# Optimization experiments

Hardware: AMD Instinct MI355X
Metric: run time of the kernel (lower is better)

## Reference

```python
import jax, jax.numpy as jnp
import numpy as np

N_HEAD = 8
D_IN = 128
D_KEY = 32
B = 65536
EPS = 1e-5
TEMP = float(D_KEY ** 0.5)


def _xavier(k, shape):
    fan_out, fan_in = shape
    limit = float(np.sqrt(6.0 / (fan_in + fan_out)))
    return jax.random.uniform(k, shape, jnp.float32, -limit, limit)


def setup_inputs() -> dict:
    key = jax.random.key(0)
    ks = jax.random.split(key, 6)
    return {
        "h_emb": jax.random.normal(ks[0], (B, D_IN), jnp.float32),
        "r_emb": jax.random.normal(ks[1], (B, D_IN), jnp.float32),
        "w_h": _xavier(ks[2], (N_HEAD * D_IN, D_IN)),
        "w_r": _xavier(ks[3], (N_HEAD * D_IN, D_IN)),
        "k_h": _xavier(ks[4], (D_KEY, D_IN)),
        "k_r": _xavier(ks[5], (D_KEY, D_IN)),
        "ln_gamma": jnp.ones((D_IN,), jnp.float32),
        "ln_beta": jnp.zeros((D_IN,), jnp.float32),
        "mode": 0,  # 0 == 'normal'
    }


def reference(h_emb, r_emb, w_h, w_r, k_h, k_r, ln_gamma, ln_beta, mode):
    # mode == 0 <=> 'normal': h_batch = h_emb.shape[0], r_batch = r_emb.shape[0]
    residual = h_emb                                     # [B, D]
    hb = h_emb.shape[0]
    rb = r_emb.shape[0]
    # linear projections to n_head copies: [1, B, H, D]
    h1 = (h_emb @ w_h.T).reshape(-1, hb, N_HEAD, D_IN)
    r1 = (r_emb @ w_r.T).reshape(-1, rb, N_HEAD, D_IN)
    # small key projections: [1, B, H, K]
    h1k = h1 @ k_h.T
    r1k = r1 @ k_r.T
    # tiny HxH attention per batch element: [1, B, H, H]
    xattn = jnp.einsum('gbhk,gbjk->gbhj', h1k / TEMP, r1k)
    g, b = xattn.shape[0], xattn.shape[1]
    xattn = jax.nn.softmax(xattn.reshape(g, b, N_HEAD * N_HEAD), axis=-1)
    xattn = xattn.reshape(g, b, N_HEAD, N_HEAD)
    h_x = xattn.sum(axis=-1)[..., None]                  # [1, B, H, 1]
    r_x = xattn.sum(axis=-2)[..., None]                  # [1, B, H, 1]
    # weighted combine + head-sum + residual: [1, B, D]
    t = (h1 * h_x + r1 * r_x).sum(axis=-2) + residual
    # LayerNorm (applied because norm_flag is False in the original)
    mu = t.mean(axis=-1, keepdims=True)
    var = ((t - mu) ** 2).mean(axis=-1, keepdims=True)
    return ln_gamma * (t - mu) / jnp.sqrt(var + EPS) + ln_beta
```

## Files before the change

### kernel.cpp

```cpp
#include <hip/hip_runtime.h>
#include <hip/hip_fp16.h>

#define TEMP_INV 0.17677669529663687f

typedef _Float16 f16x8 __attribute__((ext_vector_type(8)));
typedef float    f32x4 __attribute__((ext_vector_type(4)));

__device__ __forceinline__ ushort f2h(float x){
  __half h = __float2half(x);
  return __half_as_ushort(h);
}
__device__ __forceinline__ ushort4 f4h(float4 v){
  ushort4 o; o.x=f2h(v.x); o.y=f2h(v.y); o.z=f2h(v.z); o.w=f2h(v.w); return o;
}
__device__ __forceinline__ f16x8 cvt8(float4 a, float4 b){
  f16x8 r;
  r[0]=(_Float16)a.x; r[1]=(_Float16)a.y; r[2]=(_Float16)a.z; r[3]=(_Float16)a.w;
  r[4]=(_Float16)b.x; r[5]=(_Float16)b.y; r[6]=(_Float16)b.z; r[7]=(_Float16)b.w;
  return r;
}
__device__ __forceinline__ f16x8 vscale(f16x8 v, _Float16 s){
  f16x8 r;
  #pragma unroll
  for (int i=0;i<8;i++) r[i] = v[i]*s;
  return r;
}

__global__ void prep_kernel(const float* __restrict__ wh, const float* __restrict__ wr,
                            const float* __restrict__ kh, const float* __restrict__ kr,
                            ushort* __restrict__ w16h, ushort* __restrict__ w16r,
                            ushort* __restrict__ cwh,  ushort* __restrict__ cwr){
  if (blockIdx.x < 128){
    int t = blockIdx.x * 256 + threadIdx.x;
    int R  = t >> 5;
    int c4 = t & 31;
    int h  = R >> 7, np = R & 127;
    int kq = c4 >> 1, pos = (c4 & 1) * 4;
    int dst = ((h*16 + kq)*128 + np)*8 + pos;
    float4 a = ((const float4*)wh)[t];
    *(ushort4*)&w16h[dst] = f4h(a);
    float4 b = ((const float4*)wr)[t];
    *(ushort4*)&w16r[dst] = f4h(b);
    return;
  }
  int bid = blockIdx.x - 128;
  int m  = bid >> 5;
  int h  = (bid >> 2) & 7;
  int iq = bid & 3;
  const float* w = m ? wr : wh;
  const float* k = m ? kr : kh;
  ushort* cw = m ? cwr : cwh;

  extern __shared__ char smem[];
  float* w_s = (float*)smem;
  float* k_s = w_s + 128*32;
  int t = threadIdx.x;

  #pragma unroll
  for (int p=0;p<4;p++){
    int f = t + p*256;
    int d = f >> 3, c4 = f & 7;
    *(float4*)&w_s[d*32 + c4*4] =
        *(const float4*)&w[(size_t)(h*128 + d)*128 + iq*32 + c4*4];
  }
  #pragma unroll
  for (int p=0;p<4;p++){
    int f = t + p*256;
    ((float4*)k_s)[f] = ((const float4*)k)[f];
  }
  __syncthreads();

  int il  = t & 31;
  int kk0 = t >> 5;
  float acc[4] = {0.f,0.f,0.f,0.f};
  for (int d=0; d<128; d++){
    float wv = w_s[d*32 + il];
    #pragma unroll
    for (int j=0;j<4;j++) acc[j] += k_s[(kk0 + 8*j)*128 + d] * wv;
  }
  int i = iq*32 + il;
  #pragma unroll
  for (int j=0;j<4;j++){
    int n = h*32 + kk0 + 8*j;
    cw[(size_t)((i>>3)*256 + n)*8 + (i&7)] = f2h(acc[j]);
  }
}

__global__ __launch_bounds__(256,4) void attn16_kernel(
    const float* __restrict__ h_emb, const float* __restrict__ r_emb,
    const ushort* __restrict__ cwh,  const ushort* __restrict__ cwr,
    float* __restrict__ hx, float* __restrict__ rx)
{
  __shared__ float hk[16*292];
  __shared__ float rk[16*292];

  const int t  = threadIdx.x;
  const int b0 = blockIdx.x * 16;
  const int l  = t & 63, w = t >> 6;
  const int g  = l >> 4, c = l & 15;

  f16x8 ah[4], ar[4];
  {
    const float* ph = h_emb + ((size_t)(b0 + c))*128 + g*8;
    const float* pr = r_emb + ((size_t)(b0 + c))*128 + g*8;
    #pragma unroll
    for (int ks=0; ks<4; ks++){
      float4 lo  = *(const float4*)(ph + ks*32);
      float4 hi  = *(const float4*)(ph + ks*32 + 4);
      ah[ks] = cvt8(lo, hi);
      float4 lo2 = *(const float4*)(pr + ks*32);
      float4 hi2 = *(const float4*)(pr + ks*32 + 4);
      ar[ks] = cvt8(lo2, hi2);
    }
  }

  f32x4 aH[4] = {};
  f32x4 aR[4] = {};
  {
    const ushort* pH = cwh + ((size_t)(g*256 + w*64 + c))*8;
    const ushort* pR = cwr + ((size_t)(g*256 + w*64 + c))*8;
    #pragma unroll
    for (int ks=0; ks<4; ks++){
      #pragma unroll
      for (int nt=0; nt<4; nt++){
        f16x8 bh = *(const f16x8*)(pH + (size_t)(ks*1024 + nt*16)*8);
        f16x8 br = *(const f16x8*)(pR + (size_t)(ks*1024 + nt*16)*8);
        aH[nt] = __builtin_amdgcn_mfma_f32_16x16x32_f16(ah[ks], bh, aH[nt],0,0,0);
        aR[nt] = __builtin_amdgcn_mfma_f32_16x16x32_f16(ar[ks], br, aR[nt],0,0,0);
      }
    }
  }

  #pragma unroll
  for (int nt=0; nt<4; nt++){
    int n  = w*64 + nt*16 + c;
    int hh = n >> 5, kk = n & 31;
    #pragma unroll
    for (int reg=0; reg<4; reg++){
      int e = g*4 + reg;
      hk[e*292 + hh*36 + kk] = aH[nt][reg];
      rk[e*292 + hh*36 + kk] = aR[nt][reg];
    }
  }
  __syncthreads();

  if (t < 128){
    int e = t >> 3, hr = t & 7;
    const float* hkr = &hk[e*292 + hr*36];
    float4 hv4[8];
    #pragma unroll
    for (int q=0;q<8;q++) hv4[q] = *(const float4*)&hkr[q*4];

    float lg[8];
    #pragma unroll
    for (int j=0;j<8;j++){
      const float* rkr = &rk[e*292 + j*36];
      float s = 0.f;
      #pragma unroll
      for (int q=0;q<8;q++){
        float4 rv = *(const float4*)&rkr[q*4];
        s += hv4[q].x*rv.x + hv4[q].y*rv.y + hv4[q].z*rv.z + hv4[q].w*rv.w;
      }
      lg[j] = s * TEMP_INV;
    }
    float mx = lg[0];
    #pragma unroll
    for (int j=1;j<8;j++) mx = fmaxf(mx, lg[j]);
    mx = fmaxf(mx, __shfl_xor(mx, 1));
    mx = fmaxf(mx, __shfl_xor(mx, 2));
    mx = fmaxf(mx, __shfl_xor(mx, 4));
    float p[8]; float srow = 0.f;
    #pragma unroll
    for (int j=0;j<8;j++){ p[j] = __expf(lg[j]-mx); srow += p[j]; }
    float S = srow;
    S += __shfl_xor(S, 1); S += __shfl_xor(S, 2); S += __shfl_xor(S, 4);
    float inv = 1.0f / S;
    hx[(size_t)(b0+e)*8 + hr] = srow * inv;

    #pragma unroll
    for (int j=0;j<8;j++){
      p[j] += __shfl_xor(p[j], 1);
      p[j] += __shfl_xor(p[j], 2);
      p[j] += __shfl_xor(p[j], 4);
    }
    float cs = p[0];
    #pragma unroll
    for (int j=1;j<8;j++) cs = (hr==j) ? p[j] : cs;
    rx[(size_t)(b0+e)*8 + hr] = cs * inv;
  }
}

__global__ __launch_bounds__(256,3) void proj64_kernel(
    const float* __restrict__ h_emb, const float* __restrict__ r_emb,
    const ushort* __restrict__ w16h, const ushort* __restrict__ w16r,
    const float* __restrict__ hx, const float* __restrict__ rx,
    const float* __restrict__ gamma, const float* __restrict__ beta,
    float* __restrict__ out)
{
  __shared__ float hxs[64*12];
  __shared__ float rxs[64*12];
  __shared__ float red[64*8];

  const int t  = threadIdx.x;
  const int b0 = blockIdx.x * 64;
  const int l  = t & 63, w = t >> 6;
  const int g  = l >> 4, c = l & 15;
  const int col0 = w*32;

  if (t < 128){
    float4 v = ((const float4*)(hx + (size_t)b0*8))[t];
    *(float4*)&hxs[(t>>1)*12 + (t&1)*4] = v;
  } else {
    int t2 = t - 128;
    float4 v = ((const float4*)(rx + (size_t)b0*8))[t2];
    *(float4*)&rxs[(t2>>1)*12 + (t2&1)*4] = v;
  }
  __syncthreads();

  f32x4 tacc[4][2] = {};
  f16x8 xa[4][4];

  #pragma unroll
  for (int pass=0; pass<2; pass++){
    const float*  xsrc = pass ? r_emb : h_emb;
    const ushort* wsrc = pass ? w16r  : w16h;
    const float*  ssrc = pass ? rxs   : hxs;

    #pragma unroll
    for (int rf=0; rf<4; rf++){
      const float* p = xsrc + ((size_t)(b0 + rf*16 + c))*128 + g*8;
      #pragma unroll
      for (int ks=0; ks<4; ks++){
        float4 lo = *(const float4*)(p + ks*32);
        float4 hi = *(const float4*)(p + ks*32 + 4);
        xa[rf][ks] = cvt8(lo, hi);
      }
    }

    const ushort* bW = wsrc + ((size_t)(g*128 + col0 + c))*8;
    #pragma unroll
    for (int h=0; h<8; h++){
      _Float16 sc0 = (_Float16)ssrc[(     c)*12 + h];
      _Float16 sc1 = (_Float16)ssrc[(16 + c)*12 + h];
      _Float16 sc2 = (_Float16)ssrc[(32 + c)*12 + h];
      _Float16 sc3 = (_Float16)ssrc[(48 + c)*12 + h];
      #pragma unroll
      for (int ks=0; ks<4; ks++){
        size_t off = (size_t)((h*16 + ks*4)*128)*8;
        f16x8 b0v = *(const f16x8*)(bW + off);
        f16x8 b1v = *(const f16x8*)(bW + off + 16*8);
        f16x8 a0 = vscale(xa[0][ks], sc0);
        tacc[0][0] = __builtin_amdgcn_mfma_f32_16x16x32_f16(a0, b0v, tacc[0][0],0,0,0);
        tacc[0][1] = __builtin_amdgcn_mfma_f32_16x16x32_f16(a0, b1v, tacc[0][1],0,0,0);
        f16x8 a1 = vscale(xa[1][ks], sc1);
        tacc[1][0] = __builtin_amdgcn_mfma_f32_16x16x32_f16(a1, b0v, tacc[1][0],0,0,0);
        tacc[1][1] = __builtin_amdgcn_mfma_f32_16x16x32_f16(a1, b1v, tacc[1][1],0,0,0);
        f16x8 a2 = vscale(xa[2][ks], sc2);
        tacc[2][0] = __builtin_amdgcn_mfma_f32_16x16x32_f16(a2, b0v, tacc[2][0],0,0,0);
        tacc[2][1] = __builtin_amdgcn_mfma_f32_16x16x32_f16(a2, b1v, tacc[2][1],0,0,0);
        f16x8 a3 = vscale(xa[3][ks], sc3);
        tacc[3][0] = __builtin_amdgcn_mfma_f32_16x16x32_f16(a3, b0v, tacc[3][0],0,0,0);
        tacc[3][1] = __builtin_amdgcn_mfma_f32_16x16x32_f16(a3, b1v, tacc[3][1],0,0,0);
      }
    }
  }

  #pragma unroll
  for (int rf=0; rf<4; rf++)
    #pragma unroll
    for (int reg=0; reg<4; reg++){
      int row = rf*16 + g*4 + reg;
      const float* resid = h_emb + ((size_t)(b0+row))*128 + col0 + c;
      tacc[rf][0][reg] += resid[0];
      tacc[rf][1][reg] += resid[16];
    }

  #pragma unroll
  for (int rf=0; rf<4; rf++)
    #pragma unroll
    for (int reg=0; reg<4; reg++){
      float v0 = tacc[rf][0][reg], v1 = tacc[rf][1][reg];
      float a = v0 + v1, b2 = v0*v0 + v1*v1;
      #pragma unroll
      for (int m=1; m<16; m<<=1){
        a  += __shfl_xor(a,  m);
        b2 += __shfl_xor(b2, m);
      }
      if (c == 0){
        int row = rf*16 + g*4 + reg;
        red[row*8 + w*2]     = a;
        red[row*8 + w*2 + 1] = b2;
      }
    }
  __syncthreads();

  float gam0 = gamma[col0 + c],      bet0 = beta[col0 + c];
  float gam1 = gamma[col0 + 16 + c], bet1 = beta[col0 + 16 + c];
  #pragma unroll
  for (int rf=0; rf<4; rf++)
    #pragma unroll
    for (int reg=0; reg<4; reg++){
      int row = rf*16 + g*4 + reg;
      float S1 = red[row*8+0] + red[row*8+2] + red[row*8+4] + red[row*8+6];
      float S2 = red[row*8+1] + red[row*8+3] + red[row*8+5] + red[row*8+7];
      float mu  = S1 * 0.0078125f;
      float var = S2 * 0.0078125f - mu*mu;
      float rs  = rsqrtf(var + 1e-5f);
      float* po = out + ((size_t)(b0+row))*128 + col0 + c;
      po[0]  = gam0*((tacc[rf][0][reg]-mu)*rs) + bet0;
      po[16] = gam1*((tacc[rf][1][reg]-mu)*rs) + bet1;
    }
}

extern "C" void kernel_launch(void* const* d_in, const int* in_sizes, int n_in,
                              void* d_out, int out_size, void* d_ws, size_t ws_size,
                              hipStream_t stream){
  const float* h_emb = (const float*)d_in[0];
  const float* r_emb = (const float*)d_in[1];
  const float* w_h   = (const float*)d_in[2];
  const float* w_r   = (const float*)d_in[3];
  const float* k_h   = (const float*)d_in[4];
  const float* k_r   = (const float*)d_in[5];
  const float* gamma = (const float*)d_in[6];
  const float* beta  = (const float*)d_in[7];
  float* out = (float*)d_out;

  ushort* w16h = (ushort*)d_ws;
  ushort* w16r = w16h + 131072;
  ushort* cwh  = w16r + 131072;
  ushort* cwr  = cwh + 32768;
  float*  hxw  = (float*)(cwr + 32768);
  float*  rxw  = hxw + 524288;

  prep_kernel<<<192, 256, 32768, stream>>>(w_h, w_r, k_h, k_r,
                                           w16h, w16r, cwh, cwr);
  attn16_kernel<<<4096, 256, 0, stream>>>(h_emb, r_emb, cwh, cwr, hxw, rxw);
  proj64_kernel<<<1024, 256, 0, stream>>>(h_emb, r_emb, w16h, w16r, hxw, rxw,
                                          gamma, beta, out);
}
```

Baseline: 233.0 us.

## Stage projection weights through double-buffered LDS and retile warps to 2x2

The projection kernel now streams the fp16 weight slabs into a double-buffered shared-memory buffer with global_load_lds, prefetching the next 16 KB chunk while the current one feeds MFMAs. Before, each warp read weights straight from global/L2. Warps are also rearranged from a 1x4 column split into a 2x2 grid (32 rows x 64 columns each), so activation loads per warp halve and the LayerNorm reduction crosses only two column groups. The cost is 32 KB of LDS per block, which may limit occupancy, plus a barrier per half-head step.

```diff
diff --git a/kernel.cpp b/kernel.cpp
--- a/kernel.cpp
+++ b/kernel.cpp
@@ -24,6 +24,17 @@
   #pragma unroll
   for (int i=0;i<8;i++) r[i] = v[i]*s;
   return r;
+}
+
+__device__ __forceinline__ void stage16k(const ushort* __restrict__ gsrc,
+                                         ushort* lds, int t){
+  typedef __attribute__((address_space(1))) const unsigned int guint;
+  typedef __attribute__((address_space(3))) unsigned int luint;
+  guint* g = (guint*)gsrc;
+  luint* l = (luint*)lds;
+  #pragma unroll
+  for (int i=0;i<4;i++)
+    __builtin_amdgcn_global_load_lds(g + t*4 + i*1024, l + t*4 + i*1024, 16, 0, 0);
 }
 
 __global__ void prep_kernel(const float* __restrict__ wh, const float* __restrict__ wr,
@@ -190,22 +201,23 @@
   }
 }
 
-__global__ __launch_bounds__(256,3) void proj64_kernel(
+__global__ __launch_bounds__(256,3) void proj_kernel(
     const float* __restrict__ h_emb, const float* __restrict__ r_emb,
     const ushort* __restrict__ w16h, const ushort* __restrict__ w16r,
     const float* __restrict__ hx, const float* __restrict__ rx,
     const float* __restrict__ gamma, const float* __restrict__ beta,
     float* __restrict__ out)
 {
+  __shared__ ushort wbuf[2][8192];
   __shared__ float hxs[64*12];
   __shared__ float rxs[64*12];
-  __shared__ float red[64*8];
+  __shared__ float red[64*4];
 
   const int t  = threadIdx.x;
   const int b0 = blockIdx.x * 64;
   const int l  = t & 63, w = t >> 6;
   const int g  = l >> 4, c = l & 15;
-  const int col0 = w*32;
+  const int wm = w & 1, wn = w >> 1;
 
   if (t < 128){
     float4 v = ((const float4*)(hx + (size_t)b0*8))[t];
@@ -215,100 +227,117 @@
     float4 v = ((const float4*)(rx + (size_t)b0*8))[t2];
     *(float4*)&rxs[(t2>>1)*12 + (t2&1)*4] = v;
   }
+
+  stage16k(w16h, &wbuf[0][0], t);
   __syncthreads();
 
-  f32x4 tacc[4][2] = {};
-  f16x8 xa[4][4];
+  f32x4 tacc[2][4] = {};
 
   #pragma unroll
   for (int pass=0; pass<2; pass++){
-    const float*  xsrc = pass ? r_emb : h_emb;
-    const ushort* wsrc = pass ? w16r  : w16h;
-    const float*  ssrc = pass ? rxs   : hxs;
-
-    #pragma unroll
-    for (int rf=0; rf<4; rf++){
-      const float* p = xsrc + ((size_t)(b0 + rf*16 + c))*128 + g*8;
+    const float*  xs = pass ? r_emb : h_emb;
+    const ushort* ws = pass ? w16r  : w16h;
+    const float*  sc = pass ? rxs   : hxs;
+
+    f16x8 xa[2][4];
+    #pragma unroll
+    for (int mt=0; mt<2; mt++){
+      const float* p = xs + ((size_t)(b0 + wm*32 + mt*16 + c))*128 + g*8;
       #pragma unroll
       for (int ks=0; ks<4; ks++){
         float4 lo = *(const float4*)(p + ks*32);
         float4 hi = *(const float4*)(p + ks*32 + 4);
-        xa[rf][ks] = cvt8(lo, hi);
-      }
-    }
-
-    const ushort* bW = wsrc + ((size_t)(g*128 + col0 + c))*8;
-    #pragma unroll
+        xa[mt][ks] = cvt8(lo, hi);
+      }
+    }
+
     for (int h=0; h<8; h++){
-      _Float16 sc0 = (_Float16)ssrc[(     c)*12 + h];
-      _Float16 sc1 = (_Float16)ssrc[(16 + c)*12 + h];
-      _Float16 sc2 = (_Float16)ssrc[(32 + c)*12 + h];
-      _Float16 sc3 = (_Float16)ssrc[(48 + c)*12 + h];
+      _Float16 s0 = (_Float16)sc[(wm*32 +      c)*12 + h];
+      _Float16 s1 = (_Float16)sc[(wm*32 + 16 + c)*12 + h];
+      f16x8 a0[4], a1[4];
       #pragma unroll
       for (int ks=0; ks<4; ks++){
-        size_t off = (size_t)((h*16 + ks*4)*128)*8;
-        f16x8 b0v = *(const f16x8*)(bW + off);
-        f16x8 b1v = *(const f16x8*)(bW + off + 16*8);
-        f16x8 a0 = vscale(xa[0][ks], sc0);
-        tacc[0][0] = __builtin_amdgcn_mfma_f32_16x16x32_f16(a0, b0v, tacc[0][0],0,0,0);
-        tacc[0][1] = __builtin_amdgcn_mfma_f32_16x16x32_f16(a0, b1v, tacc[0][1],0,0,0);
-        f16x8 a1 = vscale(xa[1][ks], sc1);
-        tacc[1][0] = __builtin_amdgcn_mfma_f32_16x16x32_f16(a1, b0v, tacc[1][0],0,0,0);
-        tacc[1][1] = __builtin_amdgcn_mfma_f32_16x16x32_f16(a1, b1v, tacc[1][1],0,0,0);
-        f16x8 a2 = vscale(xa[2][ks], sc2);
-        tacc[2][0] = __builtin_amdgcn_mfma_f32_16x16x32_f16(a2, b0v, tacc[2][0],0,0,0);
-        tacc[2][1] = __builtin_amdgcn_mfma_f32_16x16x32_f16(a2, b1v, tacc[2][1],0,0,0);
-        f16x8 a3 = vscale(xa[3][ks], sc3);
-        tacc[3][0] = __builtin_amdgcn_mfma_f32_16x16x32_f16(a3, b0v, tacc[3][0],0,0,0);
-        tacc[3][1] = __builtin_amdgcn_mfma_f32_16x16x32_f16(a3, b1v, tacc[3][1],0,0,0);
-      }
-    }
-  }
-
-  #pragma unroll
-  for (int rf=0; rf<4; rf++)
+        a0[ks] = vscale(xa[0][ks], s0);
+        a1[ks] = vscale(xa[1][ks], s1);
+      }
+      #pragma unroll
+      for (int kh=0; kh<2; kh++){
+        if (!(pass==1 && h==7 && kh==1)){
+          const ushort* nsrc;
+          if (kh == 0)      nsrc = ws + (size_t)(h*16 + 8)*1024;
+          else if (h < 7)   nsrc = ws + (size_t)((h+1)*16)*1024;
+          else              nsrc = w16r;
+          stage16k(nsrc, &wbuf[kh^1][0], t);
+        }
+        const ushort* bb = &wbuf[kh][0] + (size_t)(g*128 + wn*64 + c)*8;
+        #pragma unroll
+        for (int ks2=0; ks2<2; ks2++){
+          int ks = kh*2 + ks2;
+          #pragma unroll
+          for (int nt=0; nt<4; nt++){
+            f16x8 bv = *(const f16x8*)(bb + ks2*4096 + nt*128);
+            tacc[0][nt] = __builtin_amdgcn_mfma_f32_16x16x32_f16(a0[ks], bv, tacc[0][nt],0,0,0);
+            tacc[1][nt] = __builtin_amdgcn_mfma_f32_16x16x32_f16(a1[ks], bv, tacc[1][nt],0,0,0);
+          }
+        }
+        __syncthreads();
+      }
+    }
+  }
+
+  #pragma unroll
+  for (int mt=0; mt<2; mt++)
     #pragma unroll
     for (int reg=0; reg<4; reg++){
-      int row = rf*16 + g*4 + reg;
-      const float* resid = h_emb + ((size_t)(b0+row))*128 + col0 + c;
-      tacc[rf][0][reg] += resid[0];
-      tacc[rf][1][reg] += resid[16];
-    }
-
-  #pragma unroll
-  for (int rf=0; rf<4; rf++)
+      int row = wm*32 + mt*16 + g*4 + reg;
+      const float* resid = h_emb + ((size_t)(b0+row))*128 + wn*64 + c;
+      #pragma unroll
+      for (int nt=0; nt<4; nt++)
+        tacc[mt][nt][reg] += resid[nt*16];
+    }
+
+  #pragma unroll
+  for (int mt=0; mt<2; mt++)
     #pragma unroll
     for (int reg=0; reg<4; reg++){
-      float v0 = tacc[rf][0][reg], v1 = tacc[rf][1][reg];
-      float a = v0 + v1, b2 = v0*v0 + v1*v1;
+      float a = 0.f, b2 = 0.f;
+      #pragma unroll
+      for (int nt=0; nt<4; nt++){
+        float v = tacc[mt][nt][reg]; a += v; b2 += v*v;
+      }
       #pragma unroll
       for (int m=1; m<16; m<<=1){
         a  += __shfl_xor(a,  m);
         b2 += __shfl_xor(b2, m);
       }
       if (c == 0){
-        int row = rf*16 + g*4 + reg;
-        red[row*8 + w*2]     = a;
-        red[row*8 + w*2 + 1] = b2;
+        int row = wm*32 + mt*16 + g*4 + reg;
+        red[row*4 + wn*2]     = a;
+        red[row*4 + wn*2 + 1] = b2;
       }
     }
   __syncthreads();
 
-  float gam0 = gamma[col0 + c],      bet0 = beta[col0 + c];
-  float gam1 = gamma[col0 + 16 + c], bet1 = beta[col0 + 16 + c];
-  #pragma unroll
-  for (int rf=0; rf<4; rf++)
+  float gam[4], bet[4];
+  #pragma unroll
+  for (int nt=0; nt<4; nt++){
+    gam[nt] = gamma[wn*64 + nt*16 + c];
+    bet[nt] = beta [wn*64 + nt*16 + c];
+  }
+  #pragma unroll
+  for (int mt=0; mt<2; mt++)
     #pragma unroll
     for (int reg=0; reg<4; reg++){
-      int row = rf*16 + g*4 + reg;
-      float S1 = red[row*8+0] + red[row*8+2] + red[row*8+4] + red[row*8+6];
-      float S2 = red[row*8+1] + red[row*8+3] + red[row*8+5] + red[row*8+7];
+      int row = wm*32 + mt*16 + g*4 + reg;
+      float S1 = red[row*4+0] + red[row*4+2];
+      float S2 = red[row*4+1] + red[row*4+3];
       float mu  = S1 * 0.0078125f;
       float var = S2 * 0.0078125f - mu*mu;
       float rs  = rsqrtf(var + 1e-5f);
-      float* po = out + ((size_t)(b0+row))*128 + col0 + c;
-      po[0]  = gam0*((tacc[rf][0][reg]-mu)*rs) + bet0;
-      po[16] = gam1*((tacc[rf][1][reg]-mu)*rs) + bet1;
+      float* po = out + ((size_t)(b0+row))*128 + wn*64 + c;
+      #pragma unroll
+      for (int nt=0; nt<4; nt++)
+        po[nt*16] = gam[nt]*((tacc[mt][nt][reg]-mu)*rs) + bet[nt];
     }
 }
 
@@ -335,6 +364,6 @@
   prep_kernel<<<192, 256, 32768, stream>>>(w_h, w_r, k_h, k_r,
                                            w16h, w16r, cwh, cwr);
   attn16_kernel<<<4096, 256, 0, stream>>>(h_emb, r_emb, cwh, cwr, hxw, rxw);
-  proj64_kernel<<<1024, 256, 0, stream>>>(h_emb, r_emb, w16h, w16r, hxw, rxw,
-                                          gamma, beta, out);
-}
+  proj_kernel<<<1024, 256, 0, stream>>>(h_emb, r_emb, w16h, w16r, hxw, rxw,
+                                        gamma, beta, out);
+}
```

Result: faster. 215.6 us (-7.4%).
